# Performance work log

Hardware: AMD Instinct MI355X
Metric: run time of the kernel (lower is better)

## Reference

```python
import jax, jax.numpy as jnp
import numpy as np

NEG_INF = jnp.float32(-1e30)
HASH_PRIME = jnp.int32(1000003)
BLANK_INDEX = 0
BEAM_WIDTH = 32
TOP_PATHS = 1


def _beam_search_single(logp, length):
    """CTC prefix beam search for one utterance.
    logp: [T, C] log-probabilities. length: scalar int32.
    Returns (neg_log_prob [P], lengths [P], labels [P, T]).
    """
    T, C = logp.shape
    W = BEAM_WIDTH
    classes = jnp.arange(C, dtype=jnp.int32)
    tpos = jnp.arange(T, dtype=jnp.int32)
    N = W + W * C  # stay candidates + extend candidates

    seqs0 = jnp.zeros((W, T), jnp.int32)
    lens0 = jnp.zeros((W,), jnp.int32)
    hashes0 = jnp.arange(W, dtype=jnp.int32)  # distinct -> no spurious merging
    pb0 = jnp.full((W,), NEG_INF, jnp.float32).at[0].set(0.0)  # empty prefix, ends-in-blank
    pnb0 = jnp.full((W,), NEG_INF, jnp.float32)

    def step(state, inp):
        seqs, lens, hashes, pb, pnb = state
        lp, t = inp  # lp: [C]
        last = jnp.where(lens > 0, seqs[jnp.arange(W), jnp.maximum(lens - 1, 0)], -1)
        lp_last = jnp.where(last >= 0, lp[jnp.maximum(last, 0)], NEG_INF)
        ptot = jnp.logaddexp(pb, pnb)
        # --- stay candidates (same prefix): blank emission + repeated last label
        stay_pb = ptot + lp[BLANK_INDEX]
        stay_pnb = pnb + lp_last
        # --- extend candidates (W, C): prefix + c, c != blank
        ext_pnb = jnp.where(classes[None, :] == last[:, None],
                            pb[:, None] + lp[None, :],      # repeat label needs blank gap
                            ptot[:, None] + lp[None, :])
        ext_pnb = jnp.where(classes[None, :] == BLANK_INDEX, NEG_INF, ext_pnb)
        ext_pb = jnp.full((W, C), NEG_INF, jnp.float32)
        ext_hash = hashes[:, None] * HASH_PRIME + (classes[None, :] + 1)
        cand_pb = jnp.concatenate([stay_pb, ext_pb.reshape(-1)])
        cand_pnb = jnp.concatenate([stay_pnb, ext_pnb.reshape(-1)])
        cand_hash = jnp.concatenate([hashes, ext_hash.reshape(-1)])
        # --- merge candidates sharing the same prefix (by rolling hash)
        order = jnp.argsort(cand_hash)
        h_s = cand_hash[order]
        pb_s, pnb_s = cand_pb[order], cand_pnb[order]
        new_seg = jnp.concatenate([jnp.ones((1,), jnp.int32),
                                   (h_s[1:] != h_s[:-1]).astype(jnp.int32)])
        seg_id = jnp.cumsum(new_seg) - 1

        def seg_lse(x):
            m = jax.ops.segment_max(x, seg_id, num_segments=N)
            s = jax.ops.segment_sum(jnp.exp(x - m[seg_id]), seg_id, num_segments=N)
            return m + jnp.log(s)

        pb_m = seg_lse(pb_s)[seg_id]
        pnb_m = seg_lse(pnb_s)[seg_id]
        first = new_seg == 1
        pb_s = jnp.where(first, pb_m, NEG_INF)
        pnb_s = jnp.where(first, pnb_m, NEG_INF)
        tot = jnp.logaddexp(pb_s, pnb_s)
        # --- beam pruning
        _, top_idx = jax.lax.top_k(tot, W)
        sel = order[top_idx]  # indices into flat candidate list
        is_ext = sel >= W
        parent = jnp.where(is_ext, (sel - W) // C, sel)
        cls = jnp.where(is_ext, (sel - W) % C, 0).astype(jnp.int32)
        new_pb = pb_s[top_idx]
        new_pnb = pnb_s[top_idx]
        new_hash = cand_hash[sel]
        p_seqs = seqs[parent]
        p_lens = lens[parent]
        new_seqs = jnp.where(is_ext[:, None] & (tpos[None, :] == p_lens[:, None]),
                             cls[:, None], p_seqs)
        new_lens = p_lens + is_ext.astype(jnp.int32)
        # only advance while t < data_length
        active = t < length
        seqs = jnp.where(active, new_seqs, seqs)
        lens = jnp.where(active, new_lens, lens)
        hashes = jnp.where(active, new_hash, hashes)
        pb = jnp.where(active, new_pb, pb)
        pnb = jnp.where(active, new_pnb, pnb)
        return (seqs, lens, hashes, pb, pnb), None

    (seqs, lens, hashes, pb, pnb), _ = jax.lax.scan(
        step, (seqs0, lens0, hashes0, pb0, pnb0), (logp, tpos))
    tot = jnp.logaddexp(pb, pnb)
    top_tot, top_i = jax.lax.top_k(tot, TOP_PATHS)
    return -top_tot, lens[top_i], seqs[top_i]


def setup_inputs() -> dict:
    key = jax.random.key(0)
    k1, k2 = jax.random.split(key)
    data = jax.random.normal(k1, (512, 64, 128), jnp.float32)
    data = jax.nn.log_softmax(data, axis=-1)  # layer expects log probs (from_logits=False)
    data_length = jax.random.randint(k2, (64,), 1, 513, dtype=jnp.int32)
    return {"data": data, "data_length": data_length}


def reference(data, data_length):
    # data: [max_time, batch, num_classes] log probs -> [batch, T, C]
    logp = jnp.transpose(data, (1, 0, 2))
    probs, lengths, predicted = jax.vmap(_beam_search_single)(logp, data_length)
    # top_paths == 1 path of _select_most_likely_path: plain reshape
    B = predicted.shape[0]
    T = predicted.shape[2]
    best = predicted.reshape(B, T)
    lens = lengths.reshape(B)
    # _mask_out_junk_values: fill positions >= length with blank_index
    mask = jnp.arange(T, dtype=lens.dtype)[None, :] < lens[:, None]
    return jnp.where(mask, best, jnp.int32(BLANK_INDEX))
```

## Files before the change

kernel.cpp:

```cpp
#include <hip/hip_runtime.h>
#include <stdint.h>

#define T_MAX 512
#define BATCH 64
#define NCLS  128
#define BEAM  32
#define TBL   6144
#define NEGF  (-1e30f)
#define EMPTYK ((int)0x80000000)
#define HPRIME 1000003u
#define SCAP  256

__device__ __forceinline__ float lae(float a, float b) {
  float mx = fmaxf(a, b);
  return mx + log1pf(expf(-fabsf(a - b)));
}
__device__ __forceinline__ unsigned encf(float x) {
  unsigned v = __float_as_uint(x);
  return (v & 0x80000000u) ? ~v : (v | 0x80000000u);
}
__device__ __forceinline__ float decf(unsigned u) {
  unsigned v = (u & 0x80000000u) ? (u ^ 0x80000000u) : ~u;
  return __uint_as_float(v);
}
__device__ __forceinline__ unsigned lowkey(unsigned h) {
  return 0xFFFFFFFFu - (h ^ 0x80000000u);
}

__device__ __forceinline__ int tbl_insert(int* key, int h) {
  unsigned x = (unsigned)h * 2654435761u;
  x ^= x >> 16;
  int j = (int)(((unsigned long long)x * (unsigned long long)TBL) >> 32);
  for (;;) {
    int cur = key[j];
    if (cur == EMPTYK) cur = atomicCAS(&key[j], EMPTYK, h);
    if (cur == EMPTYK || cur == h) return j;
    ++j; if (j == TBL) j = 0;
  }
}

__device__ __forceinline__ unsigned long long shflx64(unsigned long long v, int m) {
  unsigned lo = (unsigned)__shfl_xor((int)(unsigned)v, m, 64);
  unsigned hi = (unsigned)__shfl_xor((int)(unsigned)(v >> 32), m, 64);
  return ((unsigned long long)hi << 32) | lo;
}

__device__ __forceinline__ unsigned bitonic64_u32_desc(int ln, unsigned v) {
  #pragma unroll
  for (int size = 2; size <= 64; size <<= 1) {
    #pragma unroll
    for (int stride = size >> 1; stride > 0; stride >>= 1) {
      const unsigned o = (unsigned)__shfl_xor((int)v, stride, 64);
      const bool keepMax = (((ln & size) == 0) == ((ln & stride) == 0));
      v = keepMax ? (v > o ? v : o) : (v < o ? v : o);
    }
  }
  return v;
}

__global__ __launch_bounds__(512, 1)
void ctc_beam_kernel(const float* __restrict__ data,
                     const int* __restrict__ dlen,
                     int* __restrict__ out) {
  __shared__ int       tkey[TBL];
  __shared__ unsigned  tmax[TBL];
  __shared__ unsigned  tsum[TBL];
  __shared__ unsigned  tmin[TBL];
  __shared__ unsigned short bp[T_MAX * BEAM];
  __shared__ __align__(16) float lpbuf[2][NCLS];
  __shared__ int   bhash[2][BEAM];
  __shared__ float bpb[2][BEAM], bpnb[2][BEAM];
  __shared__ int   blen[2][BEAM], blast[2][BEAM];
  __shared__ float sptot[BEAM], s_pb[BEAM], s_pnb[BEAM], s_pnbm[BEAM];
  __shared__ int   stay_slot[BEAM];
  __shared__ unsigned char mergeTo[BEAM * NCLS];
  __shared__ int mergeCnt[BEAM], mergeFrom[BEAM];
  __shared__ unsigned thsub[64];
  __shared__ int anom, ovf;
  __shared__ int scnt[2];
  __shared__ unsigned long long skey[SCAP + 16];
  __shared__ unsigned sidx[SCAP];
  __shared__ unsigned long long wkey[8 * BEAM];
  __shared__ unsigned widx[8 * BEAM];
  __shared__ unsigned sel[BEAM];
  __shared__ int seqbuf[T_MAX];
  __shared__ int flen_s;

  const int tid = threadIdx.x;
  const int b = blockIdx.x;
  int L = dlen[b];
  L = L < 0 ? 0 : (L > T_MAX ? T_MAX : L);

  if (tid < BEAM) {
    bhash[0][tid] = tid;
    bpb[0][tid]   = (tid == 0) ? 0.0f : NEGF;
    bpnb[0][tid]  = NEGF;
    blen[0][tid]  = 0;
    blast[0][tid] = -1;
    mergeCnt[tid] = 0;
  }
  {
    unsigned* mtw = (unsigned*)mergeTo;
    for (int m = tid; m < (BEAM * NCLS) / 4; m += 512) mtw[m] = 0xFFFFFFFFu;
  }
  if (tid == 0) { anom = 0; ovf = 0; scnt[0] = 0; scnt[1] = 0; }
  if (tid < NCLS && L > 0) lpbuf[0][tid] = data[(size_t)b * NCLS + tid];
  __syncthreads();

  int cb = 0;
  for (int t = 0; t < L; ++t) {
    const int par = t & 1;
    const bool haspre = (tid >= 256) && (tid < 256 + NCLS) && (t + 1 < L);
    float pre = 0.0f;
    if (haspre) pre = data[((size_t)(t + 1) * BATCH + b) * NCLS + (tid - 256)];
    float* lpc = lpbuf[par];

    if (tid < BEAM) {
      const float pbv = bpb[cb][tid], pnbv = bpnb[cb][tid];
      const float pt = lae(pbv, pnbv);
      sptot[tid] = pt;
      s_pb[tid]  = pt + lpc[0];
      const int lsti = blast[cb][tid];
      s_pnb[tid] = pnbv + ((lsti >= 0) ? lpc[lsti] : NEGF);
      thsub[32 + tid] = 0u;
    }
    for (int k = tid; k < BEAM * BEAM; k += 512) {
      const int j = k >> 5, i2 = k & 31;
      const unsigned hj = (unsigned)bhash[cb][j];
      const unsigned hip = (unsigned)bhash[cb][i2] * HPRIME;
      const unsigned c = hj - hip - 1u;
      if (c < (unsigned)NCLS) {
        atomicAdd(&mergeCnt[j], 1);
        mergeFrom[j] = (i2 << 8) | (int)c;
        mergeTo[i2 * NCLS + (int)c] = (unsigned char)j;
      }
      if (j < i2) {
        const unsigned d = (hj - (unsigned)bhash[cb][i2]) * HPRIME;
        if (d + 127u <= 254u) anom = 1;
      }
    }
    __syncthreads();

    const int i  = tid >> 4;
    const int c0 = (tid & 15) << 3;
    unsigned long long k8[8];
    {
      const float pbi = bpb[cb][i];
      const float pti = sptot[i];
      const int   lsti = blast[cb][i];
      const unsigned hb = (unsigned)bhash[cb][i] * HPRIME;
      const float4 l0 = ((const float4*)(lpc + c0))[0];
      const float4 l1 = ((const float4*)(lpc + c0))[1];
      const float lv[8] = {l0.x, l0.y, l0.z, l0.w, l1.x, l1.y, l1.z, l1.w};
      const unsigned m0 = ((const unsigned*)&mergeTo[i * NCLS + c0])[0];
      const unsigned m1 = ((const unsigned*)&mergeTo[i * NCLS + c0])[1];
      unsigned pbest = 0u;
      #pragma unroll
      for (int k = 0; k < 8; ++k) {
        const int c = c0 + k;
        const unsigned mb = ((k < 4 ? (m0 >> (8 * k)) : (m1 >> (8 * (k - 4)))) & 0xFFu);
        const float x = (c == 0) ? NEGF : (((c == lsti) ? pbi : pti) + lv[k]);
        const float tot = fmaxf(x, NEGF);
        const unsigned h = hb + (unsigned)(c + 1);
        unsigned long long key =
            ((unsigned long long)encf(tot) << 32) |
            (unsigned long long)lowkey(h);
        if (mb != 0xFFu || c == 0) key = 0ull;
        k8[k] = key;
        const unsigned e32 = (unsigned)(key >> 32);
        pbest = pbest > e32 ? pbest : e32;
      }
      atomicMax(&thsub[32 + i], pbest);
    }
    if (tid < BEAM) {
      const int j = tid;
      if (mergeCnt[j] > 1) anom = 1;
      float pnbm;
      if (mergeCnt[j] == 1) {
        const int mf = mergeFrom[j];
        const int mi = mf >> 8, mc = mf & 255;
        const float e = (mc == 0) ? NEGF
            : (((mc == blast[cb][mi]) ? bpb[cb][mi] : sptot[mi]) + lpc[mc]);
        const float a = s_pnb[j];
        const float m = fmaxf(a, e);
        const float s = expf(a - m) + expf(e - m);
        pnbm = m + logf(s);
      } else {
        pnbm = s_pnb[j];
      }
      s_pnbm[j] = pnbm;
      thsub[j] = encf(lae(s_pb[j], pnbm));
    }
    if (tid == 511) scnt[par ^ 1] = 0;
    __syncthreads();

    const bool an = (anom != 0);
    bool dorare = an;
    if (!an) {
      const int ln = tid & 63;
      const unsigned sorted = bitonic64_u32_desc(ln, thsub[ln]);
      const unsigned thr = (unsigned)__shfl((int)sorted, 31, 64);

      int myn = 0;
      #pragma unroll
      for (int k = 0; k < 8; ++k) myn += ((unsigned)(k8[k] >> 32) >= thr) ? 1 : 0;
      const bool stayS = (tid < BEAM) && (thsub[tid] >= thr);
      myn += stayS ? 1 : 0;
      if (myn) {
        int o = atomicAdd(&scnt[par], myn);
        if (o + myn <= SCAP) {
          #pragma unroll
          for (int k = 0; k < 8; ++k) {
            if ((unsigned)(k8[k] >> 32) >= thr) {
              skey[o] = k8[k];
              sidx[o] = (unsigned)(BEAM + i * NCLS + (c0 + k));
              ++o;
            }
          }
          if (stayS) {
            skey[o] = ((unsigned long long)thsub[tid] << 32) |
                      (unsigned long long)lowkey((unsigned)bhash[cb][tid]);
            sidx[o] = (unsigned)tid;
          }
        } else ovf = 1;
      }
      __syncthreads();
      dorare = (ovf != 0);
    }

    if (!dorare) {
      const int scr = scnt[par];
      if (tid < scr) {
        const unsigned long long kq = skey[tid];
        int rank = 0;
        for (int p0 = 0; p0 < scr; p0 += 16) {
          #pragma unroll
          for (int pp = 0; pp < 16; ++pp) {
            const unsigned long long kp = skey[p0 + pp];
            rank += ((p0 + pp) < scr && kp > kq) ? 1 : 0;
          }
        }
        if (rank < BEAM) {
          const int j = rank;
          const unsigned s = sidx[tid];
          int nh, p, cls, ex; float npb, npnb;
          if (s < BEAM) {
            p = (int)s; cls = 0; ex = 0;
            nh = bhash[cb][p];
            npb = s_pb[p];
            npnb = s_pnbm[p];
          } else {
            const unsigned q = s - BEAM;
            p = (int)(q >> 7); cls = (int)(q & 127); ex = 1;
            nh = (int)((unsigned)bhash[cb][p] * HPRIME + (unsigned)(cls + 1));
            npb = NEGF;
            npnb = (cls == 0) ? NEGF
                 : (((cls == blast[cb][p]) ? bpb[cb][p] : sptot[p]) + lpc[cls]);
          }
          const int plen = blen[cb][p], plast = blast[cb][p];
          const int nb = cb ^ 1;
          bhash[nb][j] = nh; bpb[nb][j] = npb; bpnb[nb][j] = npnb;
          blen[nb][j]  = plen + ex;
          blast[nb][j] = ex ? cls : plast;
          bp[t * BEAM + j] = (unsigned short)(p | (cls << 5) | (ex << 12));
        }
      }
      if (tid >= 256) {
        unsigned* mtw = (unsigned*)mergeTo;
        const int base = tid - 256;
        #pragma unroll
        for (int m = 0; m < 4; ++m) mtw[base + m * 256] = 0xFFFFFFFFu;
        if (haspre) lpbuf[par ^ 1][tid - 256] = pre;
      }
      if (tid >= 64 && tid < 64 + BEAM) mergeCnt[tid - 64] = 0;
      __syncthreads();
    } else {
      for (int m = tid; m < TBL; m += 512) {
        tkey[m] = EMPTYK; tmax[m] = 0u; tsum[m] = 0u; tmin[m] = 0xFFFFFFFFu;
      }
      __syncthreads();

      int eslot[8]; float ex_[8];
      {
        const float pbi = bpb[cb][i];
        const float pti = sptot[i];
        const int   lsti = blast[cb][i];
        const unsigned hb = (unsigned)bhash[cb][i] * HPRIME;
        #pragma unroll
        for (int k = 0; k < 8; ++k) {
          const int c = c0 + k;
          int h = (int)(hb + (unsigned)(c + 1));
          if (h == EMPTYK) h = (int)0x80000001u;
          const float x = (c == 0) ? NEGF : (((c == lsti) ? pbi : pti) + lpc[c]);
          const int s = tbl_insert(tkey, h);
          atomicMax(&tmax[s], encf(x));
          atomicMin(&tmin[s], (unsigned)(BEAM + i * NCLS + c));
          eslot[k] = s; ex_[k] = x;
        }
      }
      if (tid < BEAM) {
        const int s = tbl_insert(tkey, bhash[cb][tid]);
        atomicMax(&tmax[s], encf(s_pnb[tid]));
        atomicMin(&tmin[s], (unsigned)tid);
        stay_slot[tid] = s;
      }
      __syncthreads();

      #pragma unroll
      for (int k = 0; k < 8; ++k) {
        const int s = eslot[k];
        atomicAdd((float*)&tsum[s], expf(ex_[k] - decf(tmax[s])));
      }
      if (tid < BEAM) {
        const int s = stay_slot[tid];
        atomicAdd((float*)&tsum[s], expf(s_pnb[tid] - decf(tmax[s])));
      }
      __syncthreads();

      for (int m = tid; m < TBL; m += 512) {
        if (tkey[m] != EMPTYK) {
          const float mm = decf(tmax[m]);
          const float ss = __uint_as_float(tsum[m]);
          const float pnbm = mm + logf(ss);
          tmax[m] = __float_as_uint(pnbm);
          tsum[m] = encf(lae(NEGF, pnbm));
        }
      }
      __syncthreads();
      if (tid < BEAM) {
        const int s = stay_slot[tid];
        tsum[s] = encf(lae(s_pb[tid], __uint_as_float(tmax[s])));
      }
      __syncthreads();

      {
        const int wv = tid >> 6, ln = tid & 63;
        const int base = wv * (TBL / 8) + ln * (TBL / 512);
        unsigned long long kk2[TBL / 512];
        #pragma unroll
        for (int m = 0; m < TBL / 512; ++m) {
          const int idx = base + m;
          if (tkey[idx] != EMPTYK) {
            kk2[m] = ((unsigned long long)tsum[idx] << 32) |
                     (unsigned long long)lowkey((unsigned)tkey[idx]);
          } else kk2[m] = 0ull;
        }
        unsigned cons = 0;
        for (int it = 0; it < BEAM; ++it) {
          unsigned long long best = 0ull; int bi = -1;
          #pragma unroll
          for (int m = 0; m < TBL / 512; ++m)
            if (!((cons >> m) & 1u) && kk2[m] > best) { best = kk2[m]; bi = m; }
          unsigned long long wm = best;
          #pragma unroll
          for (int off = 32; off > 0; off >>= 1) {
            const unsigned long long o = shflx64(wm, off);
            if (o > wm) wm = o;
          }
          const unsigned long long ball = __ballot(best == wm && wm != 0ull);
          const int winner = ball ? (__ffsll((long long)ball) - 1) : -1;
          if (ln == winner) {
            cons |= 1u << bi;
            wkey[wv * BEAM + it] = wm;
            widx[wv * BEAM + it] = (unsigned)(base + bi);
          } else if (winner < 0 && ln == 0) {
            wkey[wv * BEAM + it] = 0ull;
            widx[wv * BEAM + it] = 0xFFFFFFFFu;
          }
        }
      }
      __syncthreads();
      if (tid < 64) {
        unsigned long long kk2[4]; unsigned ii[4];
        #pragma unroll
        for (int m = 0; m < 4; ++m) { kk2[m] = wkey[tid * 4 + m]; ii[m] = widx[tid * 4 + m]; }
        unsigned cons = 0;
        for (int it = 0; it < BEAM; ++it) {
          unsigned long long best = 0ull; int bi = -1;
          #pragma unroll
          for (int m = 0; m < 4; ++m)
            if (!((cons >> m) & 1u) && kk2[m] > best) { best = kk2[m]; bi = m; }
          unsigned long long wm = best;
          #pragma unroll
          for (int off = 32; off > 0; off >>= 1) {
            const unsigned long long o = shflx64(wm, off);
            if (o > wm) wm = o;
          }
          const unsigned long long ball = __ballot(best == wm && wm != 0ull);
          const int winner = ball ? (__ffsll((long long)ball) - 1) : -1;
          if (tid == winner) { cons |= 1u << bi; sel[it] = ii[bi]; }
          else if (winner < 0 && tid == 0) sel[it] = 0xFFFFFFFFu;
        }
      }
      __syncthreads();

      if (tid < BEAM) {
        const int j = tid;
        const unsigned s = sel[j];
        int nh, p, cls, ex; float npb, npnb;
        if (s != 0xFFFFFFFFu) {
          nh = tkey[s];
          npnb = __uint_as_float(tmax[s]);
          npb = NEGF;
          #pragma unroll
          for (int q = 0; q < BEAM; ++q)
            if (stay_slot[q] == (int)s) npb = s_pb[q];
          const unsigned mi = tmin[s];
          ex  = (mi >= BEAM) ? 1 : 0;
          p   = ex ? (int)((mi - BEAM) >> 7) : (int)mi;
          cls = ex ? (int)((mi - BEAM) & 127) : 0;
          p &= 31;
        } else {
          nh = 0x7F000000 + j; npb = NEGF; npnb = NEGF; p = j; cls = 0; ex = 0;
        }
        const int plen = blen[cb][p], plast = blast[cb][p];
        const int nb = cb ^ 1;
        bhash[nb][j] = nh; bpb[nb][j] = npb; bpnb[nb][j] = npnb;
        blen[nb][j]  = plen + ex;
        blast[nb][j] = ex ? cls : plast;
        bp[t * BEAM + j] = (unsigned short)(p | (cls << 5) | (ex << 12));
      }
      {
        unsigned* mtw = (unsigned*)mergeTo;
        for (int m = tid; m < (BEAM * NCLS) / 4; m += 512) mtw[m] = 0xFFFFFFFFu;
      }
      if (tid >= 64 && tid < 64 + BEAM) mergeCnt[tid - 64] = 0;
      if (tid == 511) { anom = 0; ovf = 0; }
      if (haspre) lpbuf[par ^ 1][tid - 256] = pre;
      __syncthreads();
    }
    cb ^= 1;
  }

  if (tid == 0) {
    float bt = -3.4e38f; int bj = 0;
    for (int j = 0; j < BEAM; ++j) {
      const float tt = lae(bpb[cb][j], bpnb[cb][j]);
      if (tt > bt) { bt = tt; bj = j; }
    }
    int cur = bj;
    int pos = blen[cb][bj];
    flen_s = pos;
    for (int tt = L - 1; tt >= 0; --tt) {
      const unsigned short e = bp[tt * BEAM + cur];
      const int p = e & 31, cl = (e >> 5) & 127, ex = (e >> 12) & 1;
      if (ex) { --pos; if (pos >= 0) seqbuf[pos] = cl; }
      cur = p;
    }
  }
  __syncthreads();
  const int fl = flen_s;
  for (int k = tid; k < T_MAX; k += 512) {
    out[(size_t)b * T_MAX + k] = (k < fl) ? seqbuf[k] : 0;
  }
}

extern "C" void kernel_launch(void* const* d_in, const int* in_sizes, int n_in,
                              void* d_out, int out_size, void* d_ws, size_t ws_size,
                              hipStream_t stream) {
  const float* data = (const float*)d_in[0];
  const int*   dlen = (const int*)d_in[1];
  int* out = (int*)d_out;
  (void)in_sizes; (void)n_in; (void)out_size; (void)d_ws; (void)ws_size;
  hipLaunchKernelGGL(ctc_beam_kernel, dim3(BATCH), dim3(512), 0, stream,
                     data, dlen, out);
}
```

Before: 2.218 ms.

## Compute merge detection per thread in registers and drop a per-step barrier

Replaces the shared mergeTo/mergeCnt/mergeFrom tables and the 1024-pair merge scan with a per-thread loop over the 32 beam hashes. Each thread builds a bitmask of extend candidates that collide with an existing beam, and the first 32 threads count and score their own merge sources in registers. This removes one __syncthreads per time step, the shared atomics, and the table reset writes. The per-group max moves from a shared atomicMax to a wavefront shuffle reduction. In exchange every thread does 32 redundant hash compares per step and recomputes the logaddexp of its own beam.

```diff
diff --git a/kernel.cpp b/kernel.cpp
--- a/kernel.cpp
+++ b/kernel.cpp
@@ -73,8 +73,6 @@
   __shared__ int   blen[2][BEAM], blast[2][BEAM];
   __shared__ float sptot[BEAM], s_pb[BEAM], s_pnb[BEAM], s_pnbm[BEAM];
   __shared__ int   stay_slot[BEAM];
-  __shared__ unsigned char mergeTo[BEAM * NCLS];
-  __shared__ int mergeCnt[BEAM], mergeFrom[BEAM];
   __shared__ unsigned thsub[64];
   __shared__ int anom, ovf;
   __shared__ int scnt[2];
@@ -97,11 +95,6 @@
     bpnb[0][tid]  = NEGF;
     blen[0][tid]  = 0;
     blast[0][tid] = -1;
-    mergeCnt[tid] = 0;
-  }
-  {
-    unsigned* mtw = (unsigned*)mergeTo;
-    for (int m = tid; m < (BEAM * NCLS) / 4; m += 512) mtw[m] = 0xFFFFFFFFu;
   }
   if (tid == 0) { anom = 0; ovf = 0; scnt[0] = 0; scnt[1] = 0; }
   if (tid < NCLS && L > 0) lpbuf[0][tid] = data[(size_t)b * NCLS + tid];
@@ -115,81 +108,90 @@
     if (haspre) pre = data[((size_t)(t + 1) * BATCH + b) * NCLS + (tid - 256)];
     float* lpc = lpbuf[par];
 
-    if (tid < BEAM) {
-      const float pbv = bpb[cb][tid], pnbv = bpnb[cb][tid];
-      const float pt = lae(pbv, pnbv);
-      sptot[tid] = pt;
-      s_pb[tid]  = pt + lpc[0];
-      const int lsti = blast[cb][tid];
-      s_pnb[tid] = pnbv + ((lsti >= 0) ? lpc[lsti] : NEGF);
-      thsub[32 + tid] = 0u;
-    }
-    for (int k = tid; k < BEAM * BEAM; k += 512) {
-      const int j = k >> 5, i2 = k & 31;
-      const unsigned hj = (unsigned)bhash[cb][j];
-      const unsigned hip = (unsigned)bhash[cb][i2] * HPRIME;
-      const unsigned c = hj - hip - 1u;
-      if (c < (unsigned)NCLS) {
-        atomicAdd(&mergeCnt[j], 1);
-        mergeFrom[j] = (i2 << 8) | (int)c;
-        mergeTo[i2 * NCLS + (int)c] = (unsigned char)j;
-      }
-      if (j < i2) {
-        const unsigned d = (hj - (unsigned)bhash[cb][i2]) * HPRIME;
-        if (d + 127u <= 254u) anom = 1;
-      }
-    }
-    __syncthreads();
-
     const int i  = tid >> 4;
     const int c0 = (tid & 15) << 3;
+    const unsigned hb = (unsigned)bhash[cb][i] * HPRIME;
+    const float pbi = bpb[cb][i];
+    const float pti = lae(pbi, bpnb[cb][i]);
+    const int   lsti = blast[cb][i];
+    const unsigned myh = (unsigned)bhash[cb][tid & 31];
+
+    unsigned mmask = 0;
+    int anomr = 0, cnt = 0;
+    float e1 = NEGF;
+    #pragma unroll
+    for (int q = 0; q < 32; ++q) {
+      const unsigned hq = (unsigned)bhash[cb][q];
+      const unsigned rel = hq - hb - 1u - (unsigned)c0;
+      if (rel < 8u) mmask |= 1u << rel;
+      if (tid < 32) {
+        const unsigned cs = myh - hq * HPRIME - 1u;
+        if (cs < (unsigned)NCLS) {
+          if (cnt == 0) {
+            const float pbq = bpb[cb][q], pnbq = bpnb[cb][q];
+            const float ptq = lae(pbq, pnbq);
+            const int lsq = blast[cb][q];
+            e1 = (cs == 0u) ? NEGF
+               : ((((int)cs == lsq) ? pbq : ptq) + lpc[cs]);
+          }
+          ++cnt;
+        }
+        if (q != tid) {
+          const unsigned d = (myh - hq) * HPRIME;
+          if (d + 127u <= 254u) anomr = 1;
+        }
+      }
+    }
+
     unsigned long long k8[8];
     {
-      const float pbi = bpb[cb][i];
-      const float pti = sptot[i];
-      const int   lsti = blast[cb][i];
-      const unsigned hb = (unsigned)bhash[cb][i] * HPRIME;
       const float4 l0 = ((const float4*)(lpc + c0))[0];
       const float4 l1 = ((const float4*)(lpc + c0))[1];
       const float lv[8] = {l0.x, l0.y, l0.z, l0.w, l1.x, l1.y, l1.z, l1.w};
-      const unsigned m0 = ((const unsigned*)&mergeTo[i * NCLS + c0])[0];
-      const unsigned m1 = ((const unsigned*)&mergeTo[i * NCLS + c0])[1];
       unsigned pbest = 0u;
       #pragma unroll
       for (int k = 0; k < 8; ++k) {
         const int c = c0 + k;
-        const unsigned mb = ((k < 4 ? (m0 >> (8 * k)) : (m1 >> (8 * (k - 4)))) & 0xFFu);
         const float x = (c == 0) ? NEGF : (((c == lsti) ? pbi : pti) + lv[k]);
         const float tot = fmaxf(x, NEGF);
         const unsigned h = hb + (unsigned)(c + 1);
         unsigned long long key =
             ((unsigned long long)encf(tot) << 32) |
             (unsigned long long)lowkey(h);
-        if (mb != 0xFFu || c == 0) key = 0ull;
+        if (((mmask >> k) & 1u) || c == 0) key = 0ull;
         k8[k] = key;
         const unsigned e32 = (unsigned)(key >> 32);
         pbest = pbest > e32 ? pbest : e32;
       }
-      atomicMax(&thsub[32 + i], pbest);
+      #pragma unroll
+      for (int m = 1; m <= 8; m <<= 1) {
+        const unsigned o = (unsigned)__shfl_xor((int)pbest, m, 64);
+        pbest = pbest > o ? pbest : o;
+      }
+      if ((tid & 15) == 0) thsub[32 + i] = pbest;
     }
     if (tid < BEAM) {
       const int j = tid;
-      if (mergeCnt[j] > 1) anom = 1;
+      if (cnt > 1) anomr = 1;
+      const float pbv = bpb[cb][j], pnbv = bpnb[cb][j];
+      const float pt = lae(pbv, pnbv);
+      sptot[j] = pt;
+      const float spb = pt + lpc[0];
+      s_pb[j] = spb;
+      const int lstj = blast[cb][j];
+      const float spnb = pnbv + ((lstj >= 0) ? lpc[lstj] : NEGF);
+      s_pnb[j] = spnb;
       float pnbm;
-      if (mergeCnt[j] == 1) {
-        const int mf = mergeFrom[j];
-        const int mi = mf >> 8, mc = mf & 255;
-        const float e = (mc == 0) ? NEGF
-            : (((mc == blast[cb][mi]) ? bpb[cb][mi] : sptot[mi]) + lpc[mc]);
-        const float a = s_pnb[j];
-        const float m = fmaxf(a, e);
-        const float s = expf(a - m) + expf(e - m);
+      if (cnt == 1) {
+        const float m = fmaxf(spnb, e1);
+        const float s = expf(spnb - m) + expf(e1 - m);
         pnbm = m + logf(s);
       } else {
-        pnbm = s_pnb[j];
+        pnbm = spnb;
       }
       s_pnbm[j] = pnbm;
-      thsub[j] = encf(lae(s_pb[j], pnbm));
+      thsub[j] = encf(lae(spb, pnbm));
+      if (anomr) anom = 1;
     }
     if (tid == 511) scnt[par ^ 1] = 0;
     __syncthreads();
@@ -265,14 +267,7 @@
           bp[t * BEAM + j] = (unsigned short)(p | (cls << 5) | (ex << 12));
         }
       }
-      if (tid >= 256) {
-        unsigned* mtw = (unsigned*)mergeTo;
-        const int base = tid - 256;
-        #pragma unroll
-        for (int m = 0; m < 4; ++m) mtw[base + m * 256] = 0xFFFFFFFFu;
-        if (haspre) lpbuf[par ^ 1][tid - 256] = pre;
-      }
-      if (tid >= 64 && tid < 64 + BEAM) mergeCnt[tid - 64] = 0;
+      if (haspre) lpbuf[par ^ 1][tid - 256] = pre;
       __syncthreads();
     } else {
       for (int m = tid; m < TBL; m += 512) {
@@ -282,10 +277,6 @@
 
       int eslot[8]; float ex_[8];
       {
-        const float pbi = bpb[cb][i];
-        const float pti = sptot[i];
-        const int   lsti = blast[cb][i];
-        const unsigned hb = (unsigned)bhash[cb][i] * HPRIME;
         #pragma unroll
         for (int k = 0; k < 8; ++k) {
           const int c = c0 + k;
@@ -420,11 +411,6 @@
         blast[nb][j] = ex ? cls : plast;
         bp[t * BEAM + j] = (unsigned short)(p | (cls << 5) | (ex << 12));
       }
-      {
-        unsigned* mtw = (unsigned*)mergeTo;
-        for (int m = tid; m < (BEAM * NCLS) / 4; m += 512) mtw[m] = 0xFFFFFFFFu;
-      }
-      if (tid >= 64 && tid < 64 + BEAM) mergeCnt[tid - 64] = 0;
       if (tid == 511) { anom = 0; ovf = 0; }
       if (haspre) lpbuf[par ^ 1][tid - 256] = pre;
       __syncthreads();
```

New measurement: 3.674 ms. +65.7%, slower.
